# Optimization experiments

Measured on AMD Instinct MI355X. Metric: run time of the kernel, lower is better.

Reference implementation:

```python
import jax, jax.numpy as jnp
import numpy as np

D_MODEL = 1024
BATCH = 4
SEQ = 4096


def setup_inputs() -> dict:
    key = jax.random.key(0)
    kx, kwz, kwh = jax.random.split(key, 3)
    scale = 1.0 / np.sqrt(D_MODEL)
    x = jax.random.normal(kx, (BATCH, SEQ, D_MODEL), dtype=jnp.float32)
    Wz = jax.random.normal(kwz, (D_MODEL, D_MODEL), dtype=jnp.float32) * scale
    bz = jnp.zeros((D_MODEL,), dtype=jnp.float32)
    Wh = jax.random.normal(kwh, (D_MODEL, D_MODEL), dtype=jnp.float32) * scale
    bh = jnp.zeros((D_MODEL,), dtype=jnp.float32)
    return {"x": x, "Wz": Wz, "bz": bz, "Wh": Wh, "bh": bh}


def _parallel_scan_real(a, b):
    # h_t = a_t * h_{t-1} + b_t via log-depth associative scan along time axis.
    def binary_op(left, right):
        a_l, b_l = left
        a_r, b_r = right
        return (a_l * a_r, a_r * b_l + b_r)
    _, h = jax.lax.associative_scan(binary_op, (a, b), axis=1)
    return h


def reference(x, Wz, bz, Wh, bh):
    # x: [B, T, D]
    z = jax.nn.sigmoid(jnp.einsum('btd,de->bte', x, Wz) + bz)  # update gate
    h_tilde = jnp.einsum('btd,de->bte', x, Wh) + bh            # candidate
    return _parallel_scan_real(1.0 - z, z * h_tilde)           # [B, T, D]
```

## Files before the change

### kernel.cpp

```cpp
#include <hip/hip_runtime.h>
#include <hip/hip_bf16.h>
#include <stdint.h>

#define D_MODEL 1024
#define BATCH   4
#define SEQ     4096
#define M_TOTAL (BATCH*SEQ)
#define KDIM    D_MODEL
#define NTOT    2048

#define NC 128
#define CL (SEQ/NC)

#define BM 256
#define BN 256
#define BK 32
#define NT (KDIM/BK)

typedef __bf16 bf16x8 __attribute__((ext_vector_type(8)));
typedef float  f32x4  __attribute__((ext_vector_type(4)));
typedef unsigned short u16x4 __attribute__((ext_vector_type(4)));

static __device__ __forceinline__ unsigned short f2bf(float f) {
  unsigned u = __builtin_bit_cast(unsigned, f);
  u += 0x7FFFu + ((u >> 16) & 1u);
  return (unsigned short)(u >> 16);
}
static __device__ __forceinline__ float bf2f(unsigned short u) {
  return __builtin_bit_cast(float, (unsigned)u << 16);
}

__global__ __launch_bounds__(256) void k_cvt_x(const float* __restrict__ x,
                                               unsigned short* __restrict__ xb) {
  int i = blockIdx.x * 256 + threadIdx.x;
  float4 v = ((const float4*)x)[i];
  ushort4 o;
  o.x = f2bf(v.x); o.y = f2bf(v.y); o.z = f2bf(v.z); o.w = f2bf(v.w);
  ((ushort4*)xb)[i] = o;
}

__global__ void k_cvt_wT(const float* __restrict__ Wz, const float* __restrict__ Wh,
                         unsigned short* __restrict__ WzT, unsigned short* __restrict__ WhT) {
  __shared__ float tile[32][33];
  const float* W = blockIdx.z ? Wh : Wz;
  unsigned short* O = blockIdx.z ? WhT : WzT;
  int bx = blockIdx.x * 32;
  int by = blockIdx.y * 32;
  int tx = threadIdx.x, ty = threadIdx.y;
  for (int yy = ty; yy < 32; yy += 8)
    tile[yy][tx] = W[(size_t)(by + yy) * D_MODEL + bx + tx];
  __syncthreads();
  for (int yy = ty; yy < 32; yy += 8)
    O[(size_t)(bx + yy) * D_MODEL + by + tx] = f2bf(tile[tx][yy]);
}

__global__ __launch_bounds__(512, 2) void k_gemm8(
    const unsigned short* __restrict__ xb,
    const unsigned short* __restrict__ Wall,
    unsigned short* __restrict__ P, unsigned short* __restrict__ Q)
{
  __shared__ __attribute__((aligned(16))) unsigned short lds[3 * 16384];

  const int tid  = threadIdx.x;
  const int wave = tid >> 6;
  const int lane = tid & 63;
  const int m0 = blockIdx.x * BM;
  const int n0 = blockIdx.y * BN;
  const int wr = wave >> 2;
  const int wc = wave & 3;
  const int lr = lane & 15;
  const int lc = lane >> 4;

  const int p0 = wave * 2, p1 = wave * 2 + 1;
  const int c0 = p0 >> 2, rb0 = p0 & 3;
  const int c1 = p1 >> 2, rb1 = p1 & 3;

  f32x4 acc[8][4];
  #pragma unroll
  for (int i = 0; i < 8; ++i)
    #pragma unroll
    for (int j = 0; j < 4; ++j) acc[i][j] = (f32x4){0.f, 0.f, 0.f, 0.f};

  auto stage = [&](int kt, int bufb) {
    const int kb = kt * BK;
    unsigned short* ldsA = &lds[bufb * 16384];
    unsigned short* ldsB = ldsA + 8192;
    const unsigned short* a0 = xb   + (size_t)(m0 + rb0*64 + lane) * KDIM + kb + c0*8;
    const unsigned short* a1 = xb   + (size_t)(m0 + rb1*64 + lane) * KDIM + kb + c1*8;
    const unsigned short* b0 = Wall + (size_t)(n0 + rb0*64 + lane) * KDIM + kb + c0*8;
    const unsigned short* b1 = Wall + (size_t)(n0 + rb1*64 + lane) * KDIM + kb + c1*8;
    __builtin_amdgcn_global_load_lds((const __attribute__((address_space(1))) unsigned int*)a0,
        (__attribute__((address_space(3))) unsigned int*)(ldsA + (c0*256 + rb0*64)*8), 16, 0, 0);
    __builtin_amdgcn_global_load_lds((const __attribute__((address_space(1))) unsigned int*)a1,
        (__attribute__((address_space(3))) unsigned int*)(ldsA + (c1*256 + rb1*64)*8), 16, 0, 0);
    __builtin_amdgcn_global_load_lds((const __attribute__((address_space(1))) unsigned int*)b0,
        (__attribute__((address_space(3))) unsigned int*)(ldsB + (c0*256 + rb0*64)*8), 16, 0, 0);
    __builtin_amdgcn_global_load_lds((const __attribute__((address_space(1))) unsigned int*)b1,
        (__attribute__((address_space(3))) unsigned int*)(ldsB + (c1*256 + rb1*64)*8), 16, 0, 0);
  };

  stage(0, 0);
  stage(1, 1);
  asm volatile("s_waitcnt vmcnt(4)" ::: "memory");
  __builtin_amdgcn_s_barrier();

  const int aoff = (lc * 256 + wr * 128 + lr) * 8;
  const int boff = (lc * 256 + wc * 64  + lr) * 8;

  int buf = 0;
  for (int kt = 0; kt < NT; ++kt) {
    if (kt + 2 < NT) {
      int db = buf + 2; if (db >= 3) db -= 3;
      stage(kt + 2, db);
    }

    const unsigned short* bufA = &lds[buf * 16384];
    const unsigned short* bufB = bufA + 8192;

    bf16x8 bfrag[4];
    #pragma unroll
    for (int nf = 0; nf < 4; ++nf)
      bfrag[nf] = *(const bf16x8*)(bufB + boff + nf * 128);
    bf16x8 afrag[4];
    #pragma unroll
    for (int mf = 0; mf < 4; ++mf)
      afrag[mf] = *(const bf16x8*)(bufA + aoff + mf * 128);

    __builtin_amdgcn_s_setprio(1);
    #pragma unroll
    for (int mf = 0; mf < 4; ++mf)
      #pragma unroll
      for (int nf = 0; nf < 4; ++nf)
        acc[mf][nf] = __builtin_amdgcn_mfma_f32_16x16x32_bf16(afrag[mf], bfrag[nf], acc[mf][nf], 0, 0, 0);
    __builtin_amdgcn_s_setprio(0);

    #pragma unroll
    for (int mf = 0; mf < 4; ++mf)
      afrag[mf] = *(const bf16x8*)(bufA + aoff + (mf + 4) * 128);

    __builtin_amdgcn_s_setprio(1);
    #pragma unroll
    for (int mf = 0; mf < 4; ++mf)
      #pragma unroll
      for (int nf = 0; nf < 4; ++nf)
        acc[mf + 4][nf] = __builtin_amdgcn_mfma_f32_16x16x32_bf16(afrag[mf], bfrag[nf], acc[mf + 4][nf], 0, 0, 0);
    __builtin_amdgcn_s_setprio(0);

    if (kt < NT - 2) asm volatile("s_waitcnt vmcnt(4)" ::: "memory");
    else             asm volatile("s_waitcnt vmcnt(0)" ::: "memory");
    __builtin_amdgcn_s_barrier();
    buf = (buf == 2) ? 0 : buf + 1;
  }

  unsigned short* Cout = (n0 < 1024) ? P : Q;
  const int colb = (n0 < 1024) ? n0 : (n0 - 1024);
  const int cb = lane & 15;
  const int rb4 = (lane >> 4) * 4;
  #pragma unroll
  for (int mf = 0; mf < 8; ++mf) {
    #pragma unroll
    for (int nf = 0; nf < 4; ++nf) {
      const size_t col  = (size_t)(colb + wc * 64 + nf * 16 + cb);
      const size_t row0 = (size_t)(m0 + wr * 128 + mf * 16 + rb4);
      #pragma unroll
      for (int r = 0; r < 4; ++r)
        Cout[(row0 + r) * D_MODEL + col] = f2bf(acc[mf][nf][r]);
    }
  }
}

__global__ __launch_bounds__(256) void k_scan_agg(
    const unsigned short* __restrict__ P, const unsigned short* __restrict__ Q,
    const float* __restrict__ bz, const float* __restrict__ bh,
    float* __restrict__ Aagg, float* __restrict__ Bagg)
{
  int c = blockIdx.x & (NC - 1);
  int b = blockIdx.x >> 7;
  int d = threadIdx.x * 4;
  f32x4 vbz = *(const f32x4*)(bz + d);
  f32x4 vbh = *(const f32x4*)(bh + d);
  f32x4 A = {1.f, 1.f, 1.f, 1.f}, Bv = {0.f, 0.f, 0.f, 0.f};
  size_t base = ((size_t)b * SEQ + (size_t)c * CL) * D_MODEL + d;
  for (int t = 0; t < CL; ++t) {
    u16x4 pu = *(const u16x4*)(P + base + (size_t)t * D_MODEL);
    u16x4 qu = *(const u16x4*)(Q + base + (size_t)t * D_MODEL);
    #pragma unroll
    for (int r = 0; r < 4; ++r) {
      float z = 1.f / (1.f + __expf(-(bf2f(pu[r]) + vbz[r])));
      float a = 1.f - z;
      float bb = z * (bf2f(qu[r]) + vbh[r]);
      Bv[r] = a * Bv[r] + bb;
      A[r]  = a * A[r];
    }
  }
  size_t o = ((size_t)b * NC + c) * D_MODEL + d;
  *(f32x4*)(Aagg + o) = A;
  *(f32x4*)(Bagg + o) = Bv;
}

__global__ __launch_bounds__(256) void k_scan_chunks(
    const float* __restrict__ Aagg, const float* __restrict__ Bagg,
    float* __restrict__ Pref)
{
  int idx = blockIdx.x * 256 + threadIdx.x;
  int b = idx >> 10, d = idx & 1023;
  float h = 0.f;
  for (int cc = 0; cc < NC; ++cc) {
    size_t o = ((size_t)b * NC + cc) * D_MODEL + d;
    Pref[o] = h;
    h = Aagg[o] * h + Bagg[o];
  }
}

__global__ __launch_bounds__(256) void k_scan_apply(
    const unsigned short* __restrict__ P, const unsigned short* __restrict__ Q,
    const float* __restrict__ bz, const float* __restrict__ bh,
    const float* __restrict__ Pref, float* __restrict__ out)
{
  int c = blockIdx.x & (NC - 1);
  int b = blockIdx.x >> 7;
  int d = threadIdx.x * 4;
  f32x4 vbz = *(const f32x4*)(bz + d);
  f32x4 vbh = *(const f32x4*)(bh + d);
  f32x4 h = *(const f32x4*)(Pref + ((size_t)b * NC + c) * D_MODEL + d);
  size_t base = ((size_t)b * SEQ + (size_t)c * CL) * D_MODEL + d;
  for (int t = 0; t < CL; ++t) {
    u16x4 pu = *(const u16x4*)(P + base + (size_t)t * D_MODEL);
    u16x4 qu = *(const u16x4*)(Q + base + (size_t)t * D_MODEL);
    #pragma unroll
    for (int r = 0; r < 4; ++r) {
      float z = 1.f / (1.f + __expf(-(bf2f(pu[r]) + vbz[r])));
      float a = 1.f - z;
      h[r] = a * h[r] + z * (bf2f(qu[r]) + vbh[r]);
    }
    *(f32x4*)(out + base + (size_t)t * D_MODEL) = h;
  }
}

extern "C" void kernel_launch(void* const* d_in, const int* in_sizes, int n_in,
                              void* d_out, int out_size, void* d_ws, size_t ws_size,
                              hipStream_t stream)
{
  const float* x  = (const float*)d_in[0];
  const float* Wz = (const float*)d_in[1];
  const float* bz = (const float*)d_in[2];
  const float* Wh = (const float*)d_in[3];
  const float* bh = (const float*)d_in[4];

  char* ws = (char*)d_ws;
  unsigned short* xb   = (unsigned short*)(ws);
  unsigned short* Wall = (unsigned short*)(ws + 33554432);
  unsigned short* Pb   = (unsigned short*)(ws + 37748736);
  unsigned short* Qb   = (unsigned short*)(ws + 71303168);
  float* Aagg = (float*)(ws + 104857600);
  float* Bagg = (float*)(ws + 106954752);
  float* Pref = (float*)(ws + 109051904);
  float* out  = (float*)d_out;

  k_cvt_x<<<M_TOTAL * D_MODEL / 4 / 256, 256, 0, stream>>>(x, xb);
  k_cvt_wT<<<dim3(32, 32, 2), dim3(32, 8), 0, stream>>>(Wz, Wh, Wall, Wall + (size_t)1024 * 1024);
  k_gemm8<<<dim3(M_TOTAL / BM, NTOT / BN), 512, 0, stream>>>(xb, Wall, Pb, Qb);
  k_scan_agg<<<BATCH * NC, 256, 0, stream>>>(Pb, Qb, bz, bh, Aagg, Bagg);
  k_scan_chunks<<<BATCH * D_MODEL / 256, 256, 0, stream>>>(Aagg, Bagg, Pref);
  k_scan_apply<<<BATCH * NC, 256, 0, stream>>>(Pb, Qb, bz, bh, Pref, out);
}
```

Baseline: 162.4 us.

## Restructure GEMM main loop into BK=64 double-buffer with interleaved half-stage loads

Replaces the triple-buffered BK=32 pipeline with a double-buffered BK=64 scheme split into 32-wide half-tiles. Global-to-LDS loads for each A and B half-tile are issued between fragment reads and MFMA groups, with extra barriers, so loads spread across the compute phases. The goal is better overlap of memory traffic with MFMA work and fewer full-loop iterations. In exchange it uses 128KB of LDS, which may cut occupancy from two blocks per CU, and adds more barriers per iteration.

```diff
diff --git a/kernel.cpp b/kernel.cpp
--- a/kernel.cpp
+++ b/kernel.cpp
@@ -6,7 +6,7 @@
 #define BATCH   4
 #define SEQ     4096
 #define M_TOTAL (BATCH*SEQ)
-#define KDIM    D_MODEL
+#define KDIM    1024
 #define NTOT    2048
 
 #define NC 128
@@ -14,8 +14,8 @@
 
 #define BM 256
 #define BN 256
-#define BK 32
-#define NT (KDIM/BK)
+#define BK2 64
+#define NKT (KDIM/BK2)
 
 typedef __bf16 bf16x8 __attribute__((ext_vector_type(8)));
 typedef float  f32x4  __attribute__((ext_vector_type(4)));
@@ -59,7 +59,7 @@
     const unsigned short* __restrict__ Wall,
     unsigned short* __restrict__ P, unsigned short* __restrict__ Q)
 {
-  __shared__ __attribute__((aligned(16))) unsigned short lds[3 * 16384];
+  __shared__ __attribute__((aligned(16))) unsigned short lds[65536];
 
   const int tid  = threadIdx.x;
   const int wave = tid >> 6;
@@ -71,85 +71,109 @@
   const int lr = lane & 15;
   const int lc = lane >> 4;
 
-  const int p0 = wave * 2, p1 = wave * 2 + 1;
-  const int c0 = p0 >> 2, rb0 = p0 & 3;
-  const int c1 = p1 >> 2, rb1 = p1 & 3;
-
   f32x4 acc[8][4];
   #pragma unroll
   for (int i = 0; i < 8; ++i)
     #pragma unroll
     for (int j = 0; j < 4; ++j) acc[i][j] = (f32x4){0.f, 0.f, 0.f, 0.f};
 
-  auto stage = [&](int kt, int bufb) {
-    const int kb = kt * BK;
-    unsigned short* ldsA = &lds[bufb * 16384];
-    unsigned short* ldsB = ldsA + 8192;
-    const unsigned short* a0 = xb   + (size_t)(m0 + rb0*64 + lane) * KDIM + kb + c0*8;
-    const unsigned short* a1 = xb   + (size_t)(m0 + rb1*64 + lane) * KDIM + kb + c1*8;
-    const unsigned short* b0 = Wall + (size_t)(n0 + rb0*64 + lane) * KDIM + kb + c0*8;
-    const unsigned short* b1 = Wall + (size_t)(n0 + rb1*64 + lane) * KDIM + kb + c1*8;
-    __builtin_amdgcn_global_load_lds((const __attribute__((address_space(1))) unsigned int*)a0,
-        (__attribute__((address_space(3))) unsigned int*)(ldsA + (c0*256 + rb0*64)*8), 16, 0, 0);
-    __builtin_amdgcn_global_load_lds((const __attribute__((address_space(1))) unsigned int*)a1,
-        (__attribute__((address_space(3))) unsigned int*)(ldsA + (c1*256 + rb1*64)*8), 16, 0, 0);
-    __builtin_amdgcn_global_load_lds((const __attribute__((address_space(1))) unsigned int*)b0,
-        (__attribute__((address_space(3))) unsigned int*)(ldsB + (c0*256 + rb0*64)*8), 16, 0, 0);
-    __builtin_amdgcn_global_load_lds((const __attribute__((address_space(1))) unsigned int*)b1,
-        (__attribute__((address_space(3))) unsigned int*)(ldsB + (c1*256 + rb1*64)*8), 16, 0, 0);
+  auto stage = [&](const unsigned short* __restrict__ src, int rowbase,
+                   int kt, int ks, int regionShorts) {
+    #pragma unroll
+    for (int l = 0; l < 2; ++l) {
+      const int s   = l * 512 + wave * 64 + lane;
+      const int row = s & 255;
+      const int c   = s >> 8;
+      const unsigned short* g = src + (size_t)(rowbase + row) * KDIM + kt * BK2 + ks * 32 + c * 8;
+      __builtin_amdgcn_global_load_lds(
+          (const __attribute__((address_space(1))) unsigned int*)g,
+          (__attribute__((address_space(3))) unsigned int*)(lds + regionShorts + ks * 8192 + (l * 512 + wave * 64) * 8),
+          16, 0, 0);
+    }
   };
 
-  stage(0, 0);
-  stage(1, 1);
+  const int aFragBase = lc * 2048 + (wr * 128 + lr) * 8;
+  const int bFragBase = lc * 2048 + (wc * 64  + lr) * 8;
+
+  stage(xb,   m0, 0, 0, 0);
+  stage(Wall, n0, 0, 0, 16384);
+  stage(xb,   m0, 0, 1, 0);
+  stage(Wall, n0, 0, 1, 16384);
+  stage(xb,   m0, 1, 0, 32768);
+  stage(Wall, n0, 1, 0, 49152);
   asm volatile("s_waitcnt vmcnt(4)" ::: "memory");
   __builtin_amdgcn_s_barrier();
 
-  const int aoff = (lc * 256 + wr * 128 + lr) * 8;
-  const int boff = (lc * 256 + wc * 64  + lr) * 8;
-
-  int buf = 0;
-  for (int kt = 0; kt < NT; ++kt) {
-    if (kt + 2 < NT) {
-      int db = buf + 2; if (db >= 3) db -= 3;
-      stage(kt + 2, db);
-    }
-
-    const unsigned short* bufA = &lds[buf * 16384];
-    const unsigned short* bufB = bufA + 8192;
-
-    bf16x8 bfrag[4];
+  for (int kt = 0; kt < NKT; ++kt) {
+    const int buf  = (kt & 1) << 15;
+    const int nbuf = 32768 - buf;
+    bf16x8 a0[4], a1[4], b0[4];
+
     #pragma unroll
     for (int nf = 0; nf < 4; ++nf)
-      bfrag[nf] = *(const bf16x8*)(bufB + boff + nf * 128);
-    bf16x8 afrag[4];
-    #pragma unroll
-    for (int mf = 0; mf < 4; ++mf)
-      afrag[mf] = *(const bf16x8*)(bufA + aoff + mf * 128);
-
-    __builtin_amdgcn_s_setprio(1);
-    #pragma unroll
-    for (int mf = 0; mf < 4; ++mf)
-      #pragma unroll
-      for (int nf = 0; nf < 4; ++nf)
-        acc[mf][nf] = __builtin_amdgcn_mfma_f32_16x16x32_bf16(afrag[mf], bfrag[nf], acc[mf][nf], 0, 0, 0);
-    __builtin_amdgcn_s_setprio(0);
-
-    #pragma unroll
-    for (int mf = 0; mf < 4; ++mf)
-      afrag[mf] = *(const bf16x8*)(bufA + aoff + (mf + 4) * 128);
-
-    __builtin_amdgcn_s_setprio(1);
-    #pragma unroll
-    for (int mf = 0; mf < 4; ++mf)
-      #pragma unroll
-      for (int nf = 0; nf < 4; ++nf)
-        acc[mf + 4][nf] = __builtin_amdgcn_mfma_f32_16x16x32_bf16(afrag[mf], bfrag[nf], acc[mf + 4][nf], 0, 0, 0);
-    __builtin_amdgcn_s_setprio(0);
-
-    if (kt < NT - 2) asm volatile("s_waitcnt vmcnt(4)" ::: "memory");
-    else             asm volatile("s_waitcnt vmcnt(0)" ::: "memory");
-    __builtin_amdgcn_s_barrier();
-    buf = (buf == 2) ? 0 : buf + 1;
+      b0[nf] = *(const bf16x8*)(lds + buf + 16384 + bFragBase + nf * 128);
+    #pragma unroll
+    for (int mf = 0; mf < 4; ++mf)
+      a0[mf] = *(const bf16x8*)(lds + buf + aFragBase + mf * 128);
+    if (kt + 1 < NKT) stage(xb, m0, kt + 1, 1, nbuf);
+    __builtin_amdgcn_s_barrier();
+    __builtin_amdgcn_s_setprio(1);
+    #pragma unroll
+    for (int mf = 0; mf < 4; ++mf)
+      #pragma unroll
+      for (int nf = 0; nf < 4; ++nf)
+        acc[mf][nf] = __builtin_amdgcn_mfma_f32_16x16x32_bf16(a0[mf], b0[nf], acc[mf][nf], 0, 0, 0);
+    __builtin_amdgcn_s_setprio(0);
+    __builtin_amdgcn_s_barrier();
+
+    #pragma unroll
+    for (int mf = 0; mf < 4; ++mf)
+      a1[mf] = *(const bf16x8*)(lds + buf + aFragBase + (mf + 4) * 128);
+    if (kt + 1 < NKT) stage(Wall, n0, kt + 1, 1, nbuf + 16384);
+    __builtin_amdgcn_s_barrier();
+    __builtin_amdgcn_s_setprio(1);
+    #pragma unroll
+    for (int mf = 0; mf < 4; ++mf)
+      #pragma unroll
+      for (int nf = 0; nf < 4; ++nf)
+        acc[mf + 4][nf] = __builtin_amdgcn_mfma_f32_16x16x32_bf16(a1[mf], b0[nf], acc[mf + 4][nf], 0, 0, 0);
+    __builtin_amdgcn_s_setprio(0);
+    if (kt + 1 < NKT) asm volatile("s_waitcnt vmcnt(8)" ::: "memory");
+    else              asm volatile("s_waitcnt vmcnt(0)" ::: "memory");
+    __builtin_amdgcn_s_barrier();
+
+    #pragma unroll
+    for (int nf = 0; nf < 4; ++nf)
+      b0[nf] = *(const bf16x8*)(lds + buf + 16384 + 8192 + bFragBase + nf * 128);
+    #pragma unroll
+    for (int mf = 0; mf < 4; ++mf)
+      a0[mf] = *(const bf16x8*)(lds + buf + 8192 + aFragBase + mf * 128);
+    if (kt + 2 < NKT) stage(xb, m0, kt + 2, 0, buf);
+    __builtin_amdgcn_s_barrier();
+    __builtin_amdgcn_s_setprio(1);
+    #pragma unroll
+    for (int mf = 0; mf < 4; ++mf)
+      #pragma unroll
+      for (int nf = 0; nf < 4; ++nf)
+        acc[mf][nf] = __builtin_amdgcn_mfma_f32_16x16x32_bf16(a0[mf], b0[nf], acc[mf][nf], 0, 0, 0);
+    __builtin_amdgcn_s_setprio(0);
+    __builtin_amdgcn_s_barrier();
+
+    #pragma unroll
+    for (int mf = 0; mf < 4; ++mf)
+      a1[mf] = *(const bf16x8*)(lds + buf + 8192 + aFragBase + (mf + 4) * 128);
+    if (kt + 2 < NKT) stage(Wall, n0, kt + 2, 0, buf + 16384);
+    __builtin_amdgcn_s_barrier();
+    __builtin_amdgcn_s_setprio(1);
+    #pragma unroll
+    for (int mf = 0; mf < 4; ++mf)
+      #pragma unroll
+      for (int nf = 0; nf < 4; ++nf)
+        acc[mf + 4][nf] = __builtin_amdgcn_mfma_f32_16x16x32_bf16(a1[mf], b0[nf], acc[mf + 4][nf], 0, 0, 0);
+    __builtin_amdgcn_s_setprio(0);
+    if (kt + 2 < NKT)      asm volatile("s_waitcnt vmcnt(8)" ::: "memory");
+    else if (kt + 1 < NKT) asm volatile("s_waitcnt vmcnt(4)" ::: "memory");
+    __builtin_amdgcn_s_barrier();
   }
 
   unsigned short* Cout = (n0 < 1024) ? P : Q;
```

Result: slower. 172.4 us (+6.1%).

## Rewrite GEMM with 32x32x16 MFMA, BK=64, A via LDS and B in registers

Applied to the files above, without the earlier changes.

The bf16 GEMM moves from 16x16x32 to 32x32x16 MFMA with a K tile of 64 and double buffering instead of triple buffering. Only the x operand is staged through LDS. The weight fragments are loaded straight from global memory into registers one K step ahead. The C/D layout of the 32x32 MFMA lets the epilogue store four packed bf16 values per write instead of scalar stores. The goals are fewer LDS reads and barriers and wider output stores, at the cost of more register pressure and uncoalesced per-lane global loads of B.

```diff
diff --git a/kernel.cpp b/kernel.cpp
--- a/kernel.cpp
+++ b/kernel.cpp
@@ -6,7 +6,7 @@
 #define BATCH   4
 #define SEQ     4096
 #define M_TOTAL (BATCH*SEQ)
-#define KDIM    D_MODEL
+#define KDIM    1024
 #define NTOT    2048
 
 #define NC 128
@@ -14,11 +14,12 @@
 
 #define BM 256
 #define BN 256
-#define BK 32
-#define NT (KDIM/BK)
+#define BK2 64
+#define NKT (KDIM/BK2)
 
 typedef __bf16 bf16x8 __attribute__((ext_vector_type(8)));
 typedef float  f32x4  __attribute__((ext_vector_type(4)));
+typedef float  f32x16 __attribute__((ext_vector_type(16)));
 typedef unsigned short u16x4 __attribute__((ext_vector_type(4)));
 
 static __device__ __forceinline__ unsigned short f2bf(float f) {
@@ -54,12 +55,12 @@
     O[(size_t)(bx + yy) * D_MODEL + by + tx] = f2bf(tile[tx][yy]);
 }
 
-__global__ __launch_bounds__(512, 2) void k_gemm8(
+__global__ __launch_bounds__(512, 2) void k_gemm32(
     const unsigned short* __restrict__ xb,
     const unsigned short* __restrict__ Wall,
     unsigned short* __restrict__ P, unsigned short* __restrict__ Q)
 {
-  __shared__ __attribute__((aligned(16))) unsigned short lds[3 * 16384];
+  __shared__ __attribute__((aligned(16))) unsigned short ldsA[2][16384];
 
   const int tid  = threadIdx.x;
   const int wave = tid >> 6;
@@ -68,103 +69,99 @@
   const int n0 = blockIdx.y * BN;
   const int wr = wave >> 2;
   const int wc = wave & 3;
-  const int lr = lane & 15;
-  const int lc = lane >> 4;
-
-  const int p0 = wave * 2, p1 = wave * 2 + 1;
-  const int c0 = p0 >> 2, rb0 = p0 & 3;
-  const int c1 = p1 >> 2, rb1 = p1 & 3;
-
-  f32x4 acc[8][4];
+  const int l31 = lane & 31;
+  const int lh  = lane >> 5;
+
+  f32x16 acc[4][2];
   #pragma unroll
-  for (int i = 0; i < 8; ++i)
-    #pragma unroll
-    for (int j = 0; j < 4; ++j) acc[i][j] = (f32x4){0.f, 0.f, 0.f, 0.f};
-
-  auto stage = [&](int kt, int bufb) {
-    const int kb = kt * BK;
-    unsigned short* ldsA = &lds[bufb * 16384];
-    unsigned short* ldsB = ldsA + 8192;
-    const unsigned short* a0 = xb   + (size_t)(m0 + rb0*64 + lane) * KDIM + kb + c0*8;
-    const unsigned short* a1 = xb   + (size_t)(m0 + rb1*64 + lane) * KDIM + kb + c1*8;
-    const unsigned short* b0 = Wall + (size_t)(n0 + rb0*64 + lane) * KDIM + kb + c0*8;
-    const unsigned short* b1 = Wall + (size_t)(n0 + rb1*64 + lane) * KDIM + kb + c1*8;
-    __builtin_amdgcn_global_load_lds((const __attribute__((address_space(1))) unsigned int*)a0,
-        (__attribute__((address_space(3))) unsigned int*)(ldsA + (c0*256 + rb0*64)*8), 16, 0, 0);
-    __builtin_amdgcn_global_load_lds((const __attribute__((address_space(1))) unsigned int*)a1,
-        (__attribute__((address_space(3))) unsigned int*)(ldsA + (c1*256 + rb1*64)*8), 16, 0, 0);
-    __builtin_amdgcn_global_load_lds((const __attribute__((address_space(1))) unsigned int*)b0,
-        (__attribute__((address_space(3))) unsigned int*)(ldsB + (c0*256 + rb0*64)*8), 16, 0, 0);
-    __builtin_amdgcn_global_load_lds((const __attribute__((address_space(1))) unsigned int*)b1,
-        (__attribute__((address_space(3))) unsigned int*)(ldsB + (c1*256 + rb1*64)*8), 16, 0, 0);
+  for (int i = 0; i < 4; ++i)
+    #pragma unroll
+    for (int j = 0; j < 2; ++j) acc[i][j] = (f32x16){0.f};
+
+  auto stageA = [&](int kt, int b) {
+    #pragma unroll
+    for (int p = 0; p < 4; ++p) {
+      const int s   = p * 512 + tid;
+      const int row = s & 255;
+      const int kc  = s >> 8;
+      const unsigned short* g = xb + (size_t)(m0 + row) * KDIM + kt * BK2 + kc * 8;
+      __builtin_amdgcn_global_load_lds(
+          (const __attribute__((address_space(1))) unsigned int*)g,
+          (__attribute__((address_space(3))) unsigned int*)(&ldsA[b][kc * 2048 + row * 8]),
+          16, 0, 0);
+    }
   };
 
-  stage(0, 0);
-  stage(1, 1);
-  asm volatile("s_waitcnt vmcnt(4)" ::: "memory");
+  auto loadB = [&](int kt, bf16x8* bf) {
+    #pragma unroll
+    for (int nf = 0; nf < 2; ++nf)
+      #pragma unroll
+      for (int kk = 0; kk < 4; ++kk)
+        bf[nf * 4 + kk] = *(const bf16x8*)(
+            Wall + (size_t)(n0 + wc * 64 + nf * 32 + l31) * KDIM + kt * BK2 + kk * 16 + lh * 8);
+  };
+
+  stageA(0, 0);
+  __builtin_amdgcn_sched_barrier(0);
+  stageA(1, 1);
+  __builtin_amdgcn_sched_barrier(0);
+  bf16x8 breg[2][8];
+  loadB(0, breg[0]);
+  __builtin_amdgcn_sched_barrier(0);
+  asm volatile("s_waitcnt vmcnt(12)" ::: "memory");
   __builtin_amdgcn_s_barrier();
-
-  const int aoff = (lc * 256 + wr * 128 + lr) * 8;
-  const int boff = (lc * 256 + wc * 64  + lr) * 8;
-
-  int buf = 0;
-  for (int kt = 0; kt < NT; ++kt) {
-    if (kt + 2 < NT) {
-      int db = buf + 2; if (db >= 3) db -= 3;
-      stage(kt + 2, db);
-    }
-
-    const unsigned short* bufA = &lds[buf * 16384];
-    const unsigned short* bufB = bufA + 8192;
-
-    bf16x8 bfrag[4];
-    #pragma unroll
-    for (int nf = 0; nf < 4; ++nf)
-      bfrag[nf] = *(const bf16x8*)(bufB + boff + nf * 128);
-    bf16x8 afrag[4];
-    #pragma unroll
-    for (int mf = 0; mf < 4; ++mf)
-      afrag[mf] = *(const bf16x8*)(bufA + aoff + mf * 128);
-
-    __builtin_amdgcn_s_setprio(1);
-    #pragma unroll
-    for (int mf = 0; mf < 4; ++mf)
-      #pragma unroll
-      for (int nf = 0; nf < 4; ++nf)
-        acc[mf][nf] = __builtin_amdgcn_mfma_f32_16x16x32_bf16(afrag[mf], bfrag[nf], acc[mf][nf], 0, 0, 0);
-    __builtin_amdgcn_s_setprio(0);
-
-    #pragma unroll
-    for (int mf = 0; mf < 4; ++mf)
-      afrag[mf] = *(const bf16x8*)(bufA + aoff + (mf + 4) * 128);
-
-    __builtin_amdgcn_s_setprio(1);
-    #pragma unroll
-    for (int mf = 0; mf < 4; ++mf)
-      #pragma unroll
-      for (int nf = 0; nf < 4; ++nf)
-        acc[mf + 4][nf] = __builtin_amdgcn_mfma_f32_16x16x32_bf16(afrag[mf], bfrag[nf], acc[mf + 4][nf], 0, 0, 0);
-    __builtin_amdgcn_s_setprio(0);
-
-    if (kt < NT - 2) asm volatile("s_waitcnt vmcnt(4)" ::: "memory");
-    else             asm volatile("s_waitcnt vmcnt(0)" ::: "memory");
-    __builtin_amdgcn_s_barrier();
-    buf = (buf == 2) ? 0 : buf + 1;
+  __builtin_amdgcn_sched_barrier(0);
+
+  #pragma unroll
+  for (int t = 0; t < NKT; ++t) {
+    const int cur = t & 1;
+    if (t + 1 < NKT) {
+      stageA(t + 1, cur ^ 1);
+      __builtin_amdgcn_sched_barrier(0);
+      loadB(t + 1, breg[cur ^ 1]);
+      __builtin_amdgcn_sched_barrier(0);
+    }
+    #pragma unroll
+    for (int kk = 0; kk < 4; ++kk) {
+      bf16x8 af[4];
+      #pragma unroll
+      for (int mf = 0; mf < 4; ++mf)
+        af[mf] = *(const bf16x8*)(
+            &ldsA[cur][(kk * 2 + lh) * 2048 + (wr * 128 + mf * 32 + l31) * 8]);
+      __builtin_amdgcn_s_setprio(1);
+      #pragma unroll
+      for (int mf = 0; mf < 4; ++mf)
+        #pragma unroll
+        for (int nf = 0; nf < 2; ++nf)
+          acc[mf][nf] = __builtin_amdgcn_mfma_f32_32x32x16_bf16(
+              breg[cur][nf * 4 + kk], af[mf], acc[mf][nf], 0, 0, 0);
+      __builtin_amdgcn_s_setprio(0);
+    }
+    if (t + 1 < NKT) {
+      __builtin_amdgcn_sched_barrier(0);
+      asm volatile("s_waitcnt vmcnt(8)" ::: "memory");
+      __builtin_amdgcn_s_barrier();
+      __builtin_amdgcn_sched_barrier(0);
+    }
   }
 
   unsigned short* Cout = (n0 < 1024) ? P : Q;
   const int colb = (n0 < 1024) ? n0 : (n0 - 1024);
-  const int cb = lane & 15;
-  const int rb4 = (lane >> 4) * 4;
   #pragma unroll
-  for (int mf = 0; mf < 8; ++mf) {
-    #pragma unroll
-    for (int nf = 0; nf < 4; ++nf) {
-      const size_t col  = (size_t)(colb + wc * 64 + nf * 16 + cb);
-      const size_t row0 = (size_t)(m0 + wr * 128 + mf * 16 + rb4);
-      #pragma unroll
-      for (int r = 0; r < 4; ++r)
-        Cout[(row0 + r) * D_MODEL + col] = f2bf(acc[mf][nf][r]);
+  for (int mf = 0; mf < 4; ++mf) {
+    const size_t row = (size_t)(m0 + wr * 128 + mf * 32 + l31);
+    #pragma unroll
+    for (int nf = 0; nf < 2; ++nf) {
+      #pragma unroll
+      for (int g = 0; g < 4; ++g) {
+        const size_t ncol = (size_t)(colb + wc * 64 + nf * 32 + g * 8 + lh * 4);
+        u16x4 pk;
+        pk[0] = f2bf(acc[mf][nf][g * 4 + 0]);
+        pk[1] = f2bf(acc[mf][nf][g * 4 + 1]);
+        pk[2] = f2bf(acc[mf][nf][g * 4 + 2]);
+        pk[3] = f2bf(acc[mf][nf][g * 4 + 3]);
+        *(u16x4*)(Cout + row * D_MODEL + ncol) = pk;
+      }
     }
   }
 }
@@ -259,7 +256,7 @@
 
   k_cvt_x<<<M_TOTAL * D_MODEL / 4 / 256, 256, 0, stream>>>(x, xb);
   k_cvt_wT<<<dim3(32, 32, 2), dim3(32, 8), 0, stream>>>(Wz, Wh, Wall, Wall + (size_t)1024 * 1024);
-  k_gemm8<<<dim3(M_TOTAL / BM, NTOT / BN), 512, 0, stream>>>(xb, Wall, Pb, Qb);
+  k_gemm32<<<dim3(M_TOTAL / BM, NTOT / BN), 512, 0, stream>>>(xb, Wall, Pb, Qb);
   k_scan_agg<<<BATCH * NC, 256, 0, stream>>>(Pb, Qb, bz, bh, Aagg, Bagg);
   k_scan_chunks<<<BATCH * D_MODEL / 256, 256, 0, stream>>>(Aagg, Bagg, Pref);
   k_scan_apply<<<BATCH * NC, 256, 0, stream>>>(Pb, Qb, bz, bh, Pref, out);
```

Result: slower. 211.5 us (+30.2%).

## Replace pipelined 256x256 GEMM with simpler 128x128 single-buffer tile kernel

Applied to the files above, without the earlier changes.

Swaps the triple-buffered 256x256 GEMM with 8 waves for a 128x128 tile kernel using 4 waves and one LDS buffer, synchronised with __syncthreads on every k step. The MFMA operands are swapped so each lane stores four consecutive output columns as a packed 64-bit write instead of scalar 16-bit writes. The smaller tile raises the block count and occupancy, but it halves data reuse per load and drops the load/compute overlap and priority hints.

```diff
diff --git a/kernel.cpp b/kernel.cpp
--- a/kernel.cpp
+++ b/kernel.cpp
@@ -6,16 +6,16 @@
 #define BATCH   4
 #define SEQ     4096
 #define M_TOTAL (BATCH*SEQ)
-#define KDIM    D_MODEL
+#define KDIM    1024
 #define NTOT    2048
 
 #define NC 128
 #define CL (SEQ/NC)
 
-#define BM 256
-#define BN 256
-#define BK 32
-#define NT (KDIM/BK)
+#define GBM 128
+#define GBN 128
+#define GBK 32
+#define GNK (KDIM/GBK)
 
 typedef __bf16 bf16x8 __attribute__((ext_vector_type(8)));
 typedef float  f32x4  __attribute__((ext_vector_type(4)));
@@ -54,117 +54,84 @@
     O[(size_t)(bx + yy) * D_MODEL + by + tx] = f2bf(tile[tx][yy]);
 }
 
-__global__ __launch_bounds__(512, 2) void k_gemm8(
+__global__ __launch_bounds__(256, 3) void k_gemm97(
     const unsigned short* __restrict__ xb,
     const unsigned short* __restrict__ Wall,
     unsigned short* __restrict__ P, unsigned short* __restrict__ Q)
 {
-  __shared__ __attribute__((aligned(16))) unsigned short lds[3 * 16384];
+  __shared__ __attribute__((aligned(16))) unsigned short ldsA[4096];
+  __shared__ __attribute__((aligned(16))) unsigned short ldsB[4096];
 
   const int tid  = threadIdx.x;
   const int wave = tid >> 6;
   const int lane = tid & 63;
-  const int m0 = blockIdx.x * BM;
-  const int n0 = blockIdx.y * BN;
-  const int wr = wave >> 2;
-  const int wc = wave & 3;
+  const int m0 = blockIdx.x * GBM;
+  const int n0 = blockIdx.y * GBN;
+  const int wr = wave >> 1;
+  const int wc = wave & 1;
   const int lr = lane & 15;
   const int lc = lane >> 4;
 
-  const int p0 = wave * 2, p1 = wave * 2 + 1;
-  const int c0 = p0 >> 2, rb0 = p0 & 3;
-  const int c1 = p1 >> 2, rb1 = p1 & 3;
-
-  f32x4 acc[8][4];
+  f32x4 acc[4][4];
   #pragma unroll
-  for (int i = 0; i < 8; ++i)
+  for (int i = 0; i < 4; ++i)
     #pragma unroll
     for (int j = 0; j < 4; ++j) acc[i][j] = (f32x4){0.f, 0.f, 0.f, 0.f};
 
-  auto stage = [&](int kt, int bufb) {
-    const int kb = kt * BK;
-    unsigned short* ldsA = &lds[bufb * 16384];
-    unsigned short* ldsB = ldsA + 8192;
-    const unsigned short* a0 = xb   + (size_t)(m0 + rb0*64 + lane) * KDIM + kb + c0*8;
-    const unsigned short* a1 = xb   + (size_t)(m0 + rb1*64 + lane) * KDIM + kb + c1*8;
-    const unsigned short* b0 = Wall + (size_t)(n0 + rb0*64 + lane) * KDIM + kb + c0*8;
-    const unsigned short* b1 = Wall + (size_t)(n0 + rb1*64 + lane) * KDIM + kb + c1*8;
-    __builtin_amdgcn_global_load_lds((const __attribute__((address_space(1))) unsigned int*)a0,
-        (__attribute__((address_space(3))) unsigned int*)(ldsA + (c0*256 + rb0*64)*8), 16, 0, 0);
-    __builtin_amdgcn_global_load_lds((const __attribute__((address_space(1))) unsigned int*)a1,
-        (__attribute__((address_space(3))) unsigned int*)(ldsA + (c1*256 + rb1*64)*8), 16, 0, 0);
-    __builtin_amdgcn_global_load_lds((const __attribute__((address_space(1))) unsigned int*)b0,
-        (__attribute__((address_space(3))) unsigned int*)(ldsB + (c0*256 + rb0*64)*8), 16, 0, 0);
-    __builtin_amdgcn_global_load_lds((const __attribute__((address_space(1))) unsigned int*)b1,
-        (__attribute__((address_space(3))) unsigned int*)(ldsB + (c1*256 + rb1*64)*8), 16, 0, 0);
-  };
-
-  stage(0, 0);
-  stage(1, 1);
-  asm volatile("s_waitcnt vmcnt(4)" ::: "memory");
-  __builtin_amdgcn_s_barrier();
-
-  const int aoff = (lc * 256 + wr * 128 + lr) * 8;
-  const int boff = (lc * 256 + wc * 64  + lr) * 8;
-
-  int buf = 0;
-  for (int kt = 0; kt < NT; ++kt) {
-    if (kt + 2 < NT) {
-      int db = buf + 2; if (db >= 3) db -= 3;
-      stage(kt + 2, db);
-    }
-
-    const unsigned short* bufA = &lds[buf * 16384];
-    const unsigned short* bufB = bufA + 8192;
-
-    bf16x8 bfrag[4];
+  const int r0 = tid & 127, c0 = tid >> 7;
+  const int r1 = r0,        c1 = c0 + 2;
+
+  const int aoff = (lc * 128 + wr * 64 + lr) * 8;
+  const int boff = (lc * 128 + wc * 64 + lr) * 8;
+
+  for (int kt = 0; kt < GNK; ++kt) {
+    const int kb = kt * GBK;
+    __builtin_amdgcn_global_load_lds(
+        (const __attribute__((address_space(1))) unsigned int*)(xb + (size_t)(m0 + r0) * KDIM + kb + c0 * 8),
+        (__attribute__((address_space(3))) unsigned int*)(ldsA + (c0 * 128 + r0) * 8), 16, 0, 0);
+    __builtin_amdgcn_global_load_lds(
+        (const __attribute__((address_space(1))) unsigned int*)(xb + (size_t)(m0 + r1) * KDIM + kb + c1 * 8),
+        (__attribute__((address_space(3))) unsigned int*)(ldsA + (c1 * 128 + r1) * 8), 16, 0, 0);
+    __builtin_amdgcn_global_load_lds(
+        (const __attribute__((address_space(1))) unsigned int*)(Wall + (size_t)(n0 + r0) * KDIM + kb + c0 * 8),
+        (__attribute__((address_space(3))) unsigned int*)(ldsB + (c0 * 128 + r0) * 8), 16, 0, 0);
+    __builtin_amdgcn_global_load_lds(
+        (const __attribute__((address_space(1))) unsigned int*)(Wall + (size_t)(n0 + r1) * KDIM + kb + c1 * 8),
+        (__attribute__((address_space(3))) unsigned int*)(ldsB + (c1 * 128 + r1) * 8), 16, 0, 0);
+    __syncthreads();
+
+    bf16x8 afr[4], bfr[4];
     #pragma unroll
     for (int nf = 0; nf < 4; ++nf)
-      bfrag[nf] = *(const bf16x8*)(bufB + boff + nf * 128);
-    bf16x8 afrag[4];
+      bfr[nf] = *(const bf16x8*)(ldsB + boff + nf * 128);
     #pragma unroll
     for (int mf = 0; mf < 4; ++mf)
-      afrag[mf] = *(const bf16x8*)(bufA + aoff + mf * 128);
-
-    __builtin_amdgcn_s_setprio(1);
+      afr[mf] = *(const bf16x8*)(ldsA + aoff + mf * 128);
+
     #pragma unroll
     for (int mf = 0; mf < 4; ++mf)
       #pragma unroll
       for (int nf = 0; nf < 4; ++nf)
-        acc[mf][nf] = __builtin_amdgcn_mfma_f32_16x16x32_bf16(afrag[mf], bfrag[nf], acc[mf][nf], 0, 0, 0);
-    __builtin_amdgcn_s_setprio(0);
-
-    #pragma unroll
-    for (int mf = 0; mf < 4; ++mf)
-      afrag[mf] = *(const bf16x8*)(bufA + aoff + (mf + 4) * 128);
-
-    __builtin_amdgcn_s_setprio(1);
-    #pragma unroll
-    for (int mf = 0; mf < 4; ++mf)
-      #pragma unroll
-      for (int nf = 0; nf < 4; ++nf)
-        acc[mf + 4][nf] = __builtin_amdgcn_mfma_f32_16x16x32_bf16(afrag[mf], bfrag[nf], acc[mf + 4][nf], 0, 0, 0);
-    __builtin_amdgcn_s_setprio(0);
-
-    if (kt < NT - 2) asm volatile("s_waitcnt vmcnt(4)" ::: "memory");
-    else             asm volatile("s_waitcnt vmcnt(0)" ::: "memory");
-    __builtin_amdgcn_s_barrier();
-    buf = (buf == 2) ? 0 : buf + 1;
+        acc[mf][nf] = __builtin_amdgcn_mfma_f32_16x16x32_bf16(bfr[nf], afr[mf], acc[mf][nf], 0, 0, 0);
+    __syncthreads();
   }
 
   unsigned short* Cout = (n0 < 1024) ? P : Q;
   const int colb = (n0 < 1024) ? n0 : (n0 - 1024);
-  const int cb = lane & 15;
-  const int rb4 = (lane >> 4) * 4;
+  const int jm  = lane & 15;
+  const int rn4 = (lane >> 4) * 4;
   #pragma unroll
-  for (int mf = 0; mf < 8; ++mf) {
+  for (int mf = 0; mf < 4; ++mf) {
+    const size_t row = (size_t)(m0 + wr * 64 + mf * 16 + jm);
     #pragma unroll
     for (int nf = 0; nf < 4; ++nf) {
-      const size_t col  = (size_t)(colb + wc * 64 + nf * 16 + cb);
-      const size_t row0 = (size_t)(m0 + wr * 128 + mf * 16 + rb4);
-      #pragma unroll
-      for (int r = 0; r < 4; ++r)
-        Cout[(row0 + r) * D_MODEL + col] = f2bf(acc[mf][nf][r]);
+      const size_t ncol = (size_t)(colb + wc * 64 + nf * 16 + rn4);
+      u16x4 pk;
+      pk[0] = f2bf(acc[mf][nf][0]);
+      pk[1] = f2bf(acc[mf][nf][1]);
+      pk[2] = f2bf(acc[mf][nf][2]);
+      pk[3] = f2bf(acc[mf][nf][3]);
+      *(u16x4*)(Cout + row * D_MODEL + ncol) = pk;
     }
   }
 }
@@ -259,7 +226,7 @@
 
   k_cvt_x<<<M_TOTAL * D_MODEL / 4 / 256, 256, 0, stream>>>(x, xb);
   k_cvt_wT<<<dim3(32, 32, 2), dim3(32, 8), 0, stream>>>(Wz, Wh, Wall, Wall + (size_t)1024 * 1024);
-  k_gemm8<<<dim3(M_TOTAL / BM, NTOT / BN), 512, 0, stream>>>(xb, Wall, Pb, Qb);
+  k_gemm97<<<dim3(M_TOTAL / GBM, NTOT / GBN), 256, 0, stream>>>(xb, Wall, Pb, Qb);
   k_scan_agg<<<BATCH * NC, 256, 0, stream>>>(Pb, Qb, bz, bh, Aagg, Bagg);
   k_scan_chunks<<<BATCH * D_MODEL / 256, 256, 0, stream>>>(Aagg, Bagg, Pref);
   k_scan_apply<<<BATCH * NC, 256, 0, stream>>>(Pb, Qb, bz, bh, Pref, out);
```

After: 218.8 us. 1.35x slower.
